# Kernel tuning notes

Measured on AMD Instinct MI355X. Metric: run time of the kernel, lower is better.

## Reference

```python
import jax, jax.numpy as jnp
import numpy as np

IN_FEATURES = 8192
OUT_FEATURES = 8192
NNZ = 671088  # in*out*(1-0.99)
BATCH = 1024


def setup_inputs() -> dict:
    key = jax.random.key(0)
    kx, kv, kr, kc = jax.random.split(key, 4)
    x = jax.random.normal(kx, (BATCH, IN_FEATURES), dtype=jnp.float32)
    # values initialized ~ N(0,1) / sqrt(in_features), matching the module
    values = jax.random.normal(kv, (NNZ,), dtype=jnp.float32) * (1.0 / np.sqrt(IN_FEATURES))
    bias = jnp.zeros((OUT_FEATURES,), dtype=jnp.float32)
    rows = jax.random.randint(kr, (NNZ,), 0, IN_FEATURES, dtype=jnp.int32)
    cols = jax.random.randint(kc, (NNZ,), 0, OUT_FEATURES, dtype=jnp.int32)
    return {"x": x, "values": values, "bias": bias, "rows": rows, "cols": cols}


def reference(x, values, bias, rows, cols):
    # Materialize the sparse (in, out) weight via scatter-add.
    # Duplicate (row, col) pairs sum, matching torch COO .coalesce().
    W = jnp.zeros((IN_FEATURES, OUT_FEATURES), dtype=values.dtype)
    W = W.at[rows, cols].add(values)
    # res = addmm(bias, x, W) == x @ W + bias
    return x @ W + bias[None, :]
```

## Files before the change

kernel.cpp:

```cpp
#include <hip/hip_runtime.h>
#include <stdint.h>

#define IN_F   8192
#define OUT_F  8192
#define BATCH  1024
#define BT     8
#define NBT    (BATCH / BT)
#define MAIN_THREADS 1024
#define GROUPS_PER_WAVE 4
#define L_PREF 160
#define XTILE_BYTES (IN_F * 16)

typedef float f32x2 __attribute__((ext_vector_type(2)));


__device__ __forceinline__ unsigned f32_to_bf16_bits_rne(float f) {
    union { float f; unsigned u; } v; v.f = f;
    unsigned u = v.u;
    unsigned r = u + 0x7FFFu + ((u >> 16) & 1u);
    return r >> 16;
}
__device__ __forceinline__ float bf16_hi_bits_to_f32(unsigned b) {
    union { unsigned u; float f; } v; v.u = b & 0xFFFF0000u; return v.f;
}
__device__ __forceinline__ f32x2 unpack_pair(unsigned u) {
    union { unsigned u; float f; } lo, hi;
    lo.u = u << 16; hi.u = u & 0xFFFF0000u;
    f32x2 r; r.x = lo.f; r.y = hi.f; return r;
}

__global__ void scatter_kernel(const int* __restrict__ rows, const int* __restrict__ cols,
                               const float* __restrict__ vals,
                               int* __restrict__ counts, unsigned* __restrict__ ell,
                               int nnz, int L) {
    int t = blockIdx.x * blockDim.x + threadIdx.x;
    int i0 = t * 4;
    if (i0 + 3 < nnz) {
        int4   r4 = *(const int4*)(rows + i0);
        int4   c4 = *(const int4*)(cols + i0);
        float4 v4 = *(const float4*)(vals + i0);
        int c0 = c4.x, c1 = c4.y, c2 = c4.z, c3 = c4.w;
        unsigned pk0 = (f32_to_bf16_bits_rne(v4.x) << 16) | ((unsigned)r4.x << 3);
        unsigned pk1 = (f32_to_bf16_bits_rne(v4.y) << 16) | ((unsigned)r4.y << 3);
        unsigned pk2 = (f32_to_bf16_bits_rne(v4.z) << 16) | ((unsigned)r4.z << 3);
        unsigned pk3 = (f32_to_bf16_bits_rne(v4.w) << 16) | ((unsigned)r4.w << 3);
        int s0 = atomicAdd(&counts[c0], 1);
        int s1 = atomicAdd(&counts[c1], 1);
        int s2 = atomicAdd(&counts[c2], 1);
        int s3 = atomicAdd(&counts[c3], 1);
        if (s0 < L) ell[(size_t)(c0 >> 6) * (L * 64) + ((s0 >> 2) << 8) + ((c0 & 63) << 2) + (s0 & 3)] = pk0;
        if (s1 < L) ell[(size_t)(c1 >> 6) * (L * 64) + ((s1 >> 2) << 8) + ((c1 & 63) << 2) + (s1 & 3)] = pk1;
        if (s2 < L) ell[(size_t)(c2 >> 6) * (L * 64) + ((s2 >> 2) << 8) + ((c2 & 63) << 2) + (s2 & 3)] = pk2;
        if (s3 < L) ell[(size_t)(c3 >> 6) * (L * 64) + ((s3 >> 2) << 8) + ((c3 & 63) << 2) + (s3 & 3)] = pk3;
    } else {
        for (int i = i0; i < nnz; ++i) {
            int c = cols[i];
            unsigned pk = (f32_to_bf16_bits_rne(vals[i]) << 16) | ((unsigned)rows[i] << 3);
            int s = atomicAdd(&counts[c], 1);
            if (s < L)
                ell[(size_t)(c >> 6) * (L * 64) + ((s >> 2) << 8) + ((c & 63) << 2) + (s & 3)] = pk;
        }
    }
}

__device__ __forceinline__ void process_entry8(unsigned pk, const char* xbase,
                                               f32x2& a01, f32x2& a23, f32x2& a45, f32x2& a67) {
    float val = bf16_hi_bits_to_f32(pk);
    f32x2 vv; vv.x = val; vv.y = val;
    unsigned off = pk & 0xFFF8u;
    uint4 d = *(const uint4*)(xbase + off * 2);
    a01 = __builtin_elementwise_fma(unpack_pair(d.x), vv, a01);
    a23 = __builtin_elementwise_fma(unpack_pair(d.y), vv, a23);
    a45 = __builtin_elementwise_fma(unpack_pair(d.z), vv, a45);
    a67 = __builtin_elementwise_fma(unpack_pair(d.w), vv, a67);
}

__global__ __launch_bounds__(MAIN_THREADS) void spmm_kernel(
        const float* __restrict__ x,
        const float* __restrict__ bias,
        const int* __restrict__ counts,
        const unsigned* __restrict__ ell,
        float* __restrict__ out, int L) {
    extern __shared__ uint4 xl[];
    int w = blockIdx.x;
    int bt = w >> 1;
    int half = w & 1;
    int t = threadIdx.x;
    int b0 = bt * BT;

    for (int r = t; r < IN_F; r += MAIN_THREADS) {
        unsigned u0 = f32_to_bf16_bits_rne(x[(b0 + 0) * IN_F + r]);
        unsigned u1 = f32_to_bf16_bits_rne(x[(b0 + 1) * IN_F + r]);
        unsigned u2 = f32_to_bf16_bits_rne(x[(b0 + 2) * IN_F + r]);
        unsigned u3 = f32_to_bf16_bits_rne(x[(b0 + 3) * IN_F + r]);
        unsigned u4 = f32_to_bf16_bits_rne(x[(b0 + 4) * IN_F + r]);
        unsigned u5 = f32_to_bf16_bits_rne(x[(b0 + 5) * IN_F + r]);
        unsigned u6 = f32_to_bf16_bits_rne(x[(b0 + 6) * IN_F + r]);
        unsigned u7 = f32_to_bf16_bits_rne(x[(b0 + 7) * IN_F + r]);
        uint4 d;
        d.x = (u1 << 16) | u0;
        d.y = (u3 << 16) | u2;
        d.z = (u5 << 16) | u4;
        d.w = (u7 << 16) | u6;
        xl[r] = d;
    }
    __syncthreads();

    const char* xbase = (const char*)xl;
    int wave = t >> 6;
    int lane = t & 63;
    int n4cap = L >> 2;

#pragma unroll 1
    for (int it = 0; it < GROUPS_PER_WAVE; ++it) {
        int g = half * 64 + wave * GROUPS_PER_WAVE + it;
        int col = (g << 6) + lane;
        int cnt = counts[col];
#pragma unroll
        for (int off = 32; off; off >>= 1) cnt = max(cnt, __shfl_xor(cnt, off, 64));
        int n4 = (cnt + 3) >> 2;
        n4 = min(n4, n4cap);
        const uint4* ep = (const uint4*)(ell + (size_t)g * (L * 64));
        f32x2 a01 = {0.f, 0.f}, a23 = {0.f, 0.f}, a45 = {0.f, 0.f}, a67 = {0.f, 0.f};
        if (n4 > 0) {
            uint4 q = ep[lane];
#pragma unroll 1
            for (int s4 = 1; s4 < n4; ++s4) {
                uint4 qn = ep[s4 * 64 + lane];
                process_entry8(q.x, xbase, a01, a23, a45, a67);
                process_entry8(q.y, xbase, a01, a23, a45, a67);
                process_entry8(q.z, xbase, a01, a23, a45, a67);
                process_entry8(q.w, xbase, a01, a23, a45, a67);
                q = qn;
            }
            process_entry8(q.x, xbase, a01, a23, a45, a67);
            process_entry8(q.y, xbase, a01, a23, a45, a67);
            process_entry8(q.z, xbase, a01, a23, a45, a67);
            process_entry8(q.w, xbase, a01, a23, a45, a67);
        }
        float bv = bias[col];
        out[(size_t)(b0 + 0) * OUT_F + col] = a01.x + bv;
        out[(size_t)(b0 + 1) * OUT_F + col] = a01.y + bv;
        out[(size_t)(b0 + 2) * OUT_F + col] = a23.x + bv;
        out[(size_t)(b0 + 3) * OUT_F + col] = a23.y + bv;
        out[(size_t)(b0 + 4) * OUT_F + col] = a45.x + bv;
        out[(size_t)(b0 + 5) * OUT_F + col] = a45.y + bv;
        out[(size_t)(b0 + 6) * OUT_F + col] = a67.x + bv;
        out[(size_t)(b0 + 7) * OUT_F + col] = a67.y + bv;
    }
}

extern "C" void kernel_launch(void* const* d_in, const int* in_sizes, int n_in,
                              void* d_out, int out_size, void* d_ws, size_t ws_size,
                              hipStream_t stream) {
    const float* x      = (const float*)d_in[0];
    const float* values = (const float*)d_in[1];
    const float* bias   = (const float*)d_in[2];
    const int* rows = (const int*)d_in[3];
    const int* cols = (const int*)d_in[4];
    float* out = (float*)d_out;
    int nnz = in_sizes[1];

    int* counts = (int*)d_ws;
    unsigned* ell = (unsigned*)counts + 8192;

    long long cap_slots = ((long long)(ws_size / 4) - 8192) / 8192;
    int L = (int)(cap_slots & ~3LL);
    if (L > L_PREF) L = L_PREF;
    if (L < 4) L = 4;

    size_t zero_bytes = (size_t)(8192 + (size_t)L * 8192) * 4;

    static int attr_set = -1;
    if (attr_set < 0) {
        hipFuncSetAttribute((const void*)spmm_kernel,
                            hipFuncAttributeMaxDynamicSharedMemorySize, XTILE_BYTES);
        attr_set = 1;
    }

    hipMemsetAsync(d_ws, 0, zero_bytes, stream);
    int nthreads = (nnz + 3) / 4;
    scatter_kernel<<<(nthreads + 255) / 256, 256, 0, stream>>>(rows, cols, values,
                                                               counts, ell, nnz, L);
    spmm_kernel<<<NBT * 2, MAIN_THREADS, XTILE_BYTES, stream>>>(x, bias, counts, ell, out, L);
}
```

Before: 184.9 us.

## Use fp16 dot2 pairs for SpMM and pad atomic counters

Switches stored x and weight values from bf16 to fp16 so two nonzeros can be combined per v_dot2 instruction, with byte permutes interleaving the two gathered x rows. This roughly halves the FMA instruction count in the inner gather loop at the cost of extra perm instructions. It also spaces the per-column atomic counters 16 ints apart so concurrent atomics on neighbouring columns fall on separate cache lines, which enlarges the memset and shrinks the ELL capacity slightly. fp16 has a narrower range than bf16, which risks overflow or underflow for other inputs.

```diff
diff --git a/kernel.cpp b/kernel.cpp
--- a/kernel.cpp
+++ b/kernel.cpp
@@ -10,6 +10,14 @@
 #define GROUPS_PER_WAVE 4
 #define L_PREF 160
 #define XTILE_BYTES (IN_F * 16)
+#define CSTRIDE 16
+
+#if __has_builtin(__builtin_amdgcn_fdot2) && __has_builtin(__builtin_amdgcn_perm)
+#define USE_DOT2 1
+typedef _Float16 half2v __attribute__((ext_vector_type(2)));
+#else
+#define USE_DOT2 0
+#endif
 
 typedef float f32x2 __attribute__((ext_vector_type(2)));
 
@@ -28,6 +36,18 @@
     lo.u = u << 16; hi.u = u & 0xFFFF0000u;
     f32x2 r; r.x = lo.f; r.y = hi.f; return r;
 }
+
+#if USE_DOT2
+__device__ __forceinline__ unsigned val_bits(float f) {
+    return (unsigned)__builtin_bit_cast(unsigned short, (_Float16)f);
+}
+__device__ __forceinline__ unsigned x_bits(float f) {
+    return (unsigned)__builtin_bit_cast(unsigned short, (_Float16)f);
+}
+#else
+__device__ __forceinline__ unsigned val_bits(float f) { return f32_to_bf16_bits_rne(f); }
+__device__ __forceinline__ unsigned x_bits(float f)   { return f32_to_bf16_bits_rne(f); }
+#endif
 
 __global__ void scatter_kernel(const int* __restrict__ rows, const int* __restrict__ cols,
                                const float* __restrict__ vals,
@@ -40,14 +60,14 @@
         int4   c4 = *(const int4*)(cols + i0);
         float4 v4 = *(const float4*)(vals + i0);
         int c0 = c4.x, c1 = c4.y, c2 = c4.z, c3 = c4.w;
-        unsigned pk0 = (f32_to_bf16_bits_rne(v4.x) << 16) | ((unsigned)r4.x << 3);
-        unsigned pk1 = (f32_to_bf16_bits_rne(v4.y) << 16) | ((unsigned)r4.y << 3);
-        unsigned pk2 = (f32_to_bf16_bits_rne(v4.z) << 16) | ((unsigned)r4.z << 3);
-        unsigned pk3 = (f32_to_bf16_bits_rne(v4.w) << 16) | ((unsigned)r4.w << 3);
-        int s0 = atomicAdd(&counts[c0], 1);
-        int s1 = atomicAdd(&counts[c1], 1);
-        int s2 = atomicAdd(&counts[c2], 1);
-        int s3 = atomicAdd(&counts[c3], 1);
+        unsigned pk0 = (val_bits(v4.x) << 16) | ((unsigned)r4.x << 3);
+        unsigned pk1 = (val_bits(v4.y) << 16) | ((unsigned)r4.y << 3);
+        unsigned pk2 = (val_bits(v4.z) << 16) | ((unsigned)r4.z << 3);
+        unsigned pk3 = (val_bits(v4.w) << 16) | ((unsigned)r4.w << 3);
+        int s0 = atomicAdd(&counts[c0 * CSTRIDE], 1);
+        int s1 = atomicAdd(&counts[c1 * CSTRIDE], 1);
+        int s2 = atomicAdd(&counts[c2 * CSTRIDE], 1);
+        int s3 = atomicAdd(&counts[c3 * CSTRIDE], 1);
         if (s0 < L) ell[(size_t)(c0 >> 6) * (L * 64) + ((s0 >> 2) << 8) + ((c0 & 63) << 2) + (s0 & 3)] = pk0;
         if (s1 < L) ell[(size_t)(c1 >> 6) * (L * 64) + ((s1 >> 2) << 8) + ((c1 & 63) << 2) + (s1 & 3)] = pk1;
         if (s2 < L) ell[(size_t)(c2 >> 6) * (L * 64) + ((s2 >> 2) << 8) + ((c2 & 63) << 2) + (s2 & 3)] = pk2;
@@ -55,14 +75,42 @@
     } else {
         for (int i = i0; i < nnz; ++i) {
             int c = cols[i];
-            unsigned pk = (f32_to_bf16_bits_rne(vals[i]) << 16) | ((unsigned)rows[i] << 3);
-            int s = atomicAdd(&counts[c], 1);
+            unsigned pk = (val_bits(vals[i]) << 16) | ((unsigned)rows[i] << 3);
+            int s = atomicAdd(&counts[c * CSTRIDE], 1);
             if (s < L)
                 ell[(size_t)(c >> 6) * (L * 64) + ((s >> 2) << 8) + ((c & 63) << 2) + (s & 3)] = pk;
         }
     }
 }
 
+#if USE_DOT2
+__device__ __forceinline__ void process_pair8(unsigned pk0, unsigned pk1, const char* xbase,
+        float& a0, float& a1, float& a2, float& a3,
+        float& a4, float& a5, float& a6, float& a7) {
+    unsigned off0 = pk0 & 0xFFF8u;
+    unsigned off1 = pk1 & 0xFFF8u;
+    uint4 q0 = *(const uint4*)(xbase + off0 * 2);
+    uint4 q1 = *(const uint4*)(xbase + off1 * 2);
+    unsigned vv = __builtin_amdgcn_perm(pk1, pk0, 0x07060302u);
+    half2v vh = __builtin_bit_cast(half2v, vv);
+    unsigned e0 = __builtin_amdgcn_perm(q1.x, q0.x, 0x05040100u);
+    unsigned o0 = __builtin_amdgcn_perm(q1.x, q0.x, 0x07060302u);
+    unsigned e1 = __builtin_amdgcn_perm(q1.y, q0.y, 0x05040100u);
+    unsigned o1 = __builtin_amdgcn_perm(q1.y, q0.y, 0x07060302u);
+    unsigned e2 = __builtin_amdgcn_perm(q1.z, q0.z, 0x05040100u);
+    unsigned o2 = __builtin_amdgcn_perm(q1.z, q0.z, 0x07060302u);
+    unsigned e3 = __builtin_amdgcn_perm(q1.w, q0.w, 0x05040100u);
+    unsigned o3 = __builtin_amdgcn_perm(q1.w, q0.w, 0x07060302u);
+    a0 = __builtin_amdgcn_fdot2(__builtin_bit_cast(half2v, e0), vh, a0, false);
+    a1 = __builtin_amdgcn_fdot2(__builtin_bit_cast(half2v, o0), vh, a1, false);
+    a2 = __builtin_amdgcn_fdot2(__builtin_bit_cast(half2v, e1), vh, a2, false);
+    a3 = __builtin_amdgcn_fdot2(__builtin_bit_cast(half2v, o1), vh, a3, false);
+    a4 = __builtin_amdgcn_fdot2(__builtin_bit_cast(half2v, e2), vh, a4, false);
+    a5 = __builtin_amdgcn_fdot2(__builtin_bit_cast(half2v, o2), vh, a5, false);
+    a6 = __builtin_amdgcn_fdot2(__builtin_bit_cast(half2v, e3), vh, a6, false);
+    a7 = __builtin_amdgcn_fdot2(__builtin_bit_cast(half2v, o3), vh, a7, false);
+}
+#else
 __device__ __forceinline__ void process_entry8(unsigned pk, const char* xbase,
                                                f32x2& a01, f32x2& a23, f32x2& a45, f32x2& a67) {
     float val = bf16_hi_bits_to_f32(pk);
@@ -74,6 +122,7 @@
     a45 = __builtin_elementwise_fma(unpack_pair(d.z), vv, a45);
     a67 = __builtin_elementwise_fma(unpack_pair(d.w), vv, a67);
 }
+#endif
 
 __global__ __launch_bounds__(MAIN_THREADS) void spmm_kernel(
         const float* __restrict__ x,
@@ -89,14 +138,14 @@
     int b0 = bt * BT;
 
     for (int r = t; r < IN_F; r += MAIN_THREADS) {
-        unsigned u0 = f32_to_bf16_bits_rne(x[(b0 + 0) * IN_F + r]);
-        unsigned u1 = f32_to_bf16_bits_rne(x[(b0 + 1) * IN_F + r]);
-        unsigned u2 = f32_to_bf16_bits_rne(x[(b0 + 2) * IN_F + r]);
-        unsigned u3 = f32_to_bf16_bits_rne(x[(b0 + 3) * IN_F + r]);
-        unsigned u4 = f32_to_bf16_bits_rne(x[(b0 + 4) * IN_F + r]);
-        unsigned u5 = f32_to_bf16_bits_rne(x[(b0 + 5) * IN_F + r]);
-        unsigned u6 = f32_to_bf16_bits_rne(x[(b0 + 6) * IN_F + r]);
-        unsigned u7 = f32_to_bf16_bits_rne(x[(b0 + 7) * IN_F + r]);
+        unsigned u0 = x_bits(x[(b0 + 0) * IN_F + r]);
+        unsigned u1 = x_bits(x[(b0 + 1) * IN_F + r]);
+        unsigned u2 = x_bits(x[(b0 + 2) * IN_F + r]);
+        unsigned u3 = x_bits(x[(b0 + 3) * IN_F + r]);
+        unsigned u4 = x_bits(x[(b0 + 4) * IN_F + r]);
+        unsigned u5 = x_bits(x[(b0 + 5) * IN_F + r]);
+        unsigned u6 = x_bits(x[(b0 + 6) * IN_F + r]);
+        unsigned u7 = x_bits(x[(b0 + 7) * IN_F + r]);
         uint4 d;
         d.x = (u1 << 16) | u0;
         d.y = (u3 << 16) | u2;
@@ -115,12 +164,37 @@
     for (int it = 0; it < GROUPS_PER_WAVE; ++it) {
         int g = half * 64 + wave * GROUPS_PER_WAVE + it;
         int col = (g << 6) + lane;
-        int cnt = counts[col];
+        int cnt = counts[col * CSTRIDE];
 #pragma unroll
         for (int off = 32; off; off >>= 1) cnt = max(cnt, __shfl_xor(cnt, off, 64));
         int n4 = (cnt + 3) >> 2;
         n4 = min(n4, n4cap);
         const uint4* ep = (const uint4*)(ell + (size_t)g * (L * 64));
+        float bv = bias[col];
+#if USE_DOT2
+        float a0 = 0.f, a1 = 0.f, a2 = 0.f, a3 = 0.f;
+        float a4 = 0.f, a5 = 0.f, a6 = 0.f, a7 = 0.f;
+        if (n4 > 0) {
+            uint4 q = ep[lane];
+#pragma unroll 1
+            for (int s4 = 1; s4 < n4; ++s4) {
+                uint4 qn = ep[s4 * 64 + lane];
+                process_pair8(q.x, q.y, xbase, a0, a1, a2, a3, a4, a5, a6, a7);
+                process_pair8(q.z, q.w, xbase, a0, a1, a2, a3, a4, a5, a6, a7);
+                q = qn;
+            }
+            process_pair8(q.x, q.y, xbase, a0, a1, a2, a3, a4, a5, a6, a7);
+            process_pair8(q.z, q.w, xbase, a0, a1, a2, a3, a4, a5, a6, a7);
+        }
+        out[(size_t)(b0 + 0) * OUT_F + col] = a0 + bv;
+        out[(size_t)(b0 + 1) * OUT_F + col] = a1 + bv;
+        out[(size_t)(b0 + 2) * OUT_F + col] = a2 + bv;
+        out[(size_t)(b0 + 3) * OUT_F + col] = a3 + bv;
+        out[(size_t)(b0 + 4) * OUT_F + col] = a4 + bv;
+        out[(size_t)(b0 + 5) * OUT_F + col] = a5 + bv;
+        out[(size_t)(b0 + 6) * OUT_F + col] = a6 + bv;
+        out[(size_t)(b0 + 7) * OUT_F + col] = a7 + bv;
+#else
         f32x2 a01 = {0.f, 0.f}, a23 = {0.f, 0.f}, a45 = {0.f, 0.f}, a67 = {0.f, 0.f};
         if (n4 > 0) {
             uint4 q = ep[lane];
@@ -138,7 +212,6 @@
             process_entry8(q.z, xbase, a01, a23, a45, a67);
             process_entry8(q.w, xbase, a01, a23, a45, a67);
         }
-        float bv = bias[col];
         out[(size_t)(b0 + 0) * OUT_F + col] = a01.x + bv;
         out[(size_t)(b0 + 1) * OUT_F + col] = a01.y + bv;
         out[(size_t)(b0 + 2) * OUT_F + col] = a23.x + bv;
@@ -147,6 +220,7 @@
         out[(size_t)(b0 + 5) * OUT_F + col] = a45.y + bv;
         out[(size_t)(b0 + 6) * OUT_F + col] = a67.x + bv;
         out[(size_t)(b0 + 7) * OUT_F + col] = a67.y + bv;
+#endif
     }
 }
 
@@ -162,14 +236,14 @@
     int nnz = in_sizes[1];
 
     int* counts = (int*)d_ws;
-    unsigned* ell = (unsigned*)counts + 8192;
-
-    long long cap_slots = ((long long)(ws_size / 4) - 8192) / 8192;
+    unsigned* ell = (unsigned*)counts + 8192 * CSTRIDE;
+
+    long long cap_slots = ((long long)(ws_size / 4) - 8192LL * CSTRIDE) / 8192;
     int L = (int)(cap_slots & ~3LL);
     if (L > L_PREF) L = L_PREF;
     if (L < 4) L = 4;
 
-    size_t zero_bytes = (size_t)(8192 + (size_t)L * 8192) * 4;
+    size_t zero_bytes = (size_t)(8192 * CSTRIDE + (size_t)L * 8192) * 4;
 
     static int attr_set = -1;
     if (attr_set < 0) {
```

New measurement: 176.7 us. 1.05x faster.
